# Performance work log

Measured on AMD Instinct MI355X. Metric: run time of the kernel, lower is better.

## Reference

```python
import jax, jax.numpy as jnp
import numpy as np

N_NODES = 20000
N_EDGES = 640000
HIDDEN = 128
HEADS = 8
HEAD_DIM = HIDDEN // HEADS
SCALE = HEAD_DIM ** -0.5
EPS = 1e-8


def setup_inputs() -> dict:
    key = jax.random.key(0)
    ks = jax.random.split(key, 12)
    s = HIDDEN ** -0.5
    return {
        "query": jax.random.normal(ks[0], (N_NODES, HIDDEN), jnp.float32),
        "key": jax.random.normal(ks[1], (N_NODES, HIDDEN), jnp.float32),
        "value": jax.random.normal(ks[2], (N_NODES, HIDDEN), jnp.float32),
        "edge_index": jax.random.randint(ks[3], (2, N_EDGES), 0, N_NODES, jnp.int64 if jax.config.jax_enable_x64 else jnp.int32),
        "Wq": jax.random.normal(ks[4], (HIDDEN, HIDDEN), jnp.float32) * s,
        "bq": jax.random.normal(ks[5], (HIDDEN,), jnp.float32) * s,
        "Wk": jax.random.normal(ks[6], (HIDDEN, HIDDEN), jnp.float32) * s,
        "bk": jax.random.normal(ks[7], (HIDDEN,), jnp.float32) * s,
        "Wv": jax.random.normal(ks[8], (HIDDEN, HIDDEN), jnp.float32) * s,
        "bv": jax.random.normal(ks[9], (HIDDEN,), jnp.float32) * s,
        "Wo": jax.random.normal(ks[10], (HIDDEN, HIDDEN), jnp.float32) * s,
        "bo": jax.random.normal(ks[11], (HIDDEN,), jnp.float32) * s,
    }


def reference(query, key, value, edge_index, Wq, bq, Wk, bk, Wv, bv, Wo, bo):
    n = query.shape[0]
    # projections (torch nn.Linear: x @ W.T + b)
    Q = (query @ Wq.T + bq).reshape(n, HEADS, HEAD_DIM)
    K = (key @ Wk.T + bk).reshape(n, HEADS, HEAD_DIM)
    V = (value @ Wv.T + bv).reshape(n, HEADS, HEAD_DIM)

    src, dst = edge_index[0], edge_index[1]
    # per-edge, per-head scores: [E, H]
    scores = jnp.einsum('ehd,ehd->eh', Q[dst], K[src]) * SCALE
    # segment softmax over incoming edges of each dst node
    seg_max = jax.ops.segment_max(scores, dst, num_segments=n)  # [N, H]
    seg_max = jnp.where(jnp.isfinite(seg_max), seg_max, 0.0)
    exp_scores = jnp.exp(scores - seg_max[dst])
    seg_sum = jax.ops.segment_sum(exp_scores, dst, num_segments=n)  # [N, H]
    attn = exp_scores / (seg_sum[dst] + EPS)  # [E, H]

    # scatter-weighted aggregation of V[src] into dst
    weighted = attn[:, :, None] * V[src]  # [E, H, D]
    out = jax.ops.segment_sum(weighted, dst, num_segments=n)  # [N, H, D]
    out = out.reshape(n, HIDDEN)
    return out @ Wo.T + bo
```

## Files before the change

kernel.cpp:

```cpp
#include <hip/hip_runtime.h>
#include <math.h>

#define NN 20000
#define NE 640000
#define HID 128
#define NH 8
#define HD 16
#define ATT_SCALE 0.25f

#define EPB 4096
#define NBLK1 157
#define NBUCK 157
#define SCAN_N (NBUCK * NBLK1)
#define SPT 25
#define PCHUNK 79

typedef __attribute__((ext_vector_type(8))) short bhalf8;
typedef __attribute__((ext_vector_type(4))) float floatx4;

#if defined(__has_builtin)
#if __has_builtin(__builtin_amdgcn_fdot2_f32_bf16)
#define USE_BF16_DOT2 1
#endif
#endif

__device__ __forceinline__ short f2b(float f) {
  union { float f; unsigned u; } a;
  a.f = f;
  unsigned r = a.u + 0x7FFF + ((a.u >> 16) & 1);
  return (short)(r >> 16);
}

__device__ __forceinline__ float b2f(short s) {
  union { unsigned u; float f; } a;
  a.u = ((unsigned)(unsigned short)s) << 16;
  return a.f;
}

#ifdef USE_BF16_DOT2
typedef __attribute__((ext_vector_type(2))) __bf16 bf16x2;
__device__ __forceinline__ bf16x2 asbf2(unsigned x) {
  union { unsigned u; bf16x2 v; } c;
  c.u = x;
  return c.v;
}
__device__ __forceinline__ float dot8(const bhalf8& k, const bhalf8& q) {
  const unsigned* kp = (const unsigned*)&k;
  const unsigned* qp = (const unsigned*)&q;
  float d = 0.f;
#pragma unroll
  for (int u = 0; u < 4; ++u)
    d = __builtin_amdgcn_fdot2_f32_bf16(asbf2(kp[u]), asbf2(qp[u]), d, false);
  return d;
}
#else
__device__ __forceinline__ float dot8(const bhalf8& k, const bhalf8& q) {
  float d = 0.f;
#pragma unroll
  for (int u = 0; u < 8; ++u) d += b2f(k[u]) * b2f(q[u]);
  return d;
}
#endif

__device__ __forceinline__ bhalf8 load_a8(const float* __restrict__ p) {
  float4 x0 = *(const float4*)p;
  float4 x1 = *(const float4*)(p + 4);
  bhalf8 a;
  a[0] = f2b(x0.x); a[1] = f2b(x0.y); a[2] = f2b(x0.z); a[3] = f2b(x0.w);
  a[4] = f2b(x1.x); a[5] = f2b(x1.y); a[6] = f2b(x1.z); a[7] = f2b(x1.w);
  return a;
}

__global__ __launch_bounds__(256) void k_hist_wconv(
    const int* __restrict__ dst, int* __restrict__ cnt1,
    const float* __restrict__ W0, const float* __restrict__ W1,
    const float* __restrict__ W2, const float* __restrict__ W3,
    short* __restrict__ out) {
  int t = threadIdx.x, b = blockIdx.x;
  if (b < NBLK1) {
    __shared__ int h[NBUCK];
    for (int i = t; i < NBUCK; i += 256) h[i] = 0;
    __syncthreads();
    const int4* d4 = (const int4*)dst;
    int q0 = (b * EPB) >> 2;
#pragma unroll
    for (int it = 0; it < EPB / 1024; ++it) {
      int i4 = q0 + it * 256 + t;
      if (i4 < NE / 4) {
        int4 d = d4[i4];
        atomicAdd(&h[d.x >> 7], 1);
        atomicAdd(&h[d.y >> 7], 1);
        atomicAdd(&h[d.z >> 7], 1);
        atomicAdd(&h[d.w >> 7], 1);
      }
    }
    __syncthreads();
    for (int i = t; i < NBUCK; i += 256) cnt1[i * NBLK1 + b] = h[i];
  } else {
    int i = (b - NBLK1) * 1024 + t * 4;
    int m = i >> 14;
    const float* src = (m == 0) ? W0 : (m == 1) ? W1 : (m == 2) ? W2 : W3;
    float4 x = *(const float4*)(src + (i & 16383));
    short4 o;
    o.x = f2b(x.x); o.y = f2b(x.y); o.z = f2b(x.z); o.w = f2b(x.w);
    *(short4*)(out + i) = o;
  }
}

template <int STRIDE, int HALF>
__device__ __forceinline__ void gemm_mfma(const float* __restrict__ X,
                                          const short* __restrict__ Wb,
                                          const float* __restrict__ B,
                                          short* __restrict__ O, int wrow) {
  int lane = threadIdx.x & 63;
  int rr = lane & 15;
  int g = lane >> 4;
  int arow = wrow + rr;
  floatx4 acc[8];
#pragma unroll
  for (int nt = 0; nt < 8; ++nt) acc[nt] = (floatx4){0.f, 0.f, 0.f, 0.f};
#pragma unroll
  for (int kt = 0; kt < 4; ++kt) {
    bhalf8 a;
    if (arow < NN) {
      a = load_a8(X + (size_t)arow * HID + kt * 32 + g * 8);
    } else {
      a = (bhalf8){0, 0, 0, 0, 0, 0, 0, 0};
    }
#pragma unroll
    for (int nt = 0; nt < 8; ++nt) {
      bhalf8 b = *(const bhalf8*)(Wb + (nt * 16 + rr) * HID + kt * 32 + g * 8);
      acc[nt] = __builtin_amdgcn_mfma_f32_16x16x32_bf16(a, b, acc[nt], 0, 0, 0);
    }
  }
  int orow0 = wrow + g * 4;
#pragma unroll
  for (int nt = 0; nt < 8; ++nt) {
    int col = nt * 16 + rr;
    float bias = B[col];
#pragma unroll
    for (int i = 0; i < 4; ++i) {
      int r = orow0 + i;
      if (r < NN) {
        O[((size_t)(nt >> 1) * NN + r) * STRIDE + HALF + (nt & 1) * 16 + rr] =
            f2b(acc[nt][i] + bias);
      }
    }
  }
}

__global__ __launch_bounds__(1024) void k_scan_proj(
    int* __restrict__ cnt1, int* __restrict__ boff,
    const float* __restrict__ q, const float* __restrict__ k,
    const float* __restrict__ v, const short* __restrict__ Wb,
    const float* __restrict__ bq, const float* __restrict__ bk,
    const float* __restrict__ bv, short* __restrict__ Qh,
    short* __restrict__ KVh) {
  __shared__ int sa[1024], sb[1024];
  int t = threadIdx.x;
  if (blockIdx.x == 0) {
    int base = t * SPT;
    int s = 0;
#pragma unroll 5
    for (int u = 0; u < SPT; ++u) {
      int i = base + u;
      s += (i < SCAN_N) ? cnt1[i] : 0;
    }
    sa[t] = s;
    __syncthreads();
    int* sp = sa;
    int* dp = sb;
    for (int st = 1; st < 1024; st <<= 1) {
      dp[t] = sp[t] + (t >= st ? sp[t - st] : 0);
      __syncthreads();
      int* tmp = sp; sp = dp; dp = tmp;
    }
    int run = sp[t] - s;
#pragma unroll 5
    for (int u = 0; u < SPT; ++u) {
      int i = base + u;
      if (i < SCAN_N) {
        int vv = cnt1[i];
        cnt1[i] = run;
        run += vv;
      }
    }
    __syncthreads();
    for (int i = t; i < NBUCK; i += 1024) boff[i] = cnt1[i * NBLK1];
    if (t == 0) boff[NBUCK] = NE;
  } else {
    int b = blockIdx.x - 1;
    int mat = b / PCHUNK;
    int wrow = (b % PCHUNK) * 256 + (t >> 6) * 16;
    if (mat == 0) gemm_mfma<32, 0>(q, Wb, bq, Qh, wrow);
    else if (mat == 1) gemm_mfma<64, 0>(k, Wb + 16384, bk, KVh, wrow);
    else gemm_mfma<64, 32>(v, Wb + 2 * 16384, bv, KVh, wrow);
  }
}

__global__ __launch_bounds__(256) void k_p1scat(const int* __restrict__ src,
                                                const int* __restrict__ dst,
                                                const int* __restrict__ cnt1,
                                                int* __restrict__ tmp) {
  __shared__ int cur[NBUCK];
  int t = threadIdx.x, b = blockIdx.x;
  for (int i = t; i < NBUCK; i += 256) cur[i] = cnt1[i * NBLK1 + b];
  __syncthreads();
  const int4* s4 = (const int4*)src;
  const int4* d4 = (const int4*)dst;
  int q0 = (b * EPB) >> 2;
#pragma unroll
  for (int it = 0; it < EPB / 1024; ++it) {
    int i4 = q0 + it * 256 + t;
    if (i4 < NE / 4) {
      int4 s = s4[i4];
      int4 d = d4[i4];
      int p;
      p = atomicAdd(&cur[d.x >> 7], 1); tmp[p] = (s.x << 7) | (d.x & 127);
      p = atomicAdd(&cur[d.y >> 7], 1); tmp[p] = (s.y << 7) | (d.y & 127);
      p = atomicAdd(&cur[d.z >> 7], 1); tmp[p] = (s.z << 7) | (d.z & 127);
      p = atomicAdd(&cur[d.w >> 7], 1); tmp[p] = (s.w << 7) | (d.w & 127);
    }
  }
}

__global__ __launch_bounds__(128, 4) void k_edge(
    const int* __restrict__ tmp, const int* __restrict__ boff,
    const short* __restrict__ Qh, const short* __restrict__ KVh,
    const short* __restrict__ Wb, const float* __restrict__ bo,
    float* __restrict__ O) {
  __shared__ int hits[512];
  __shared__ int els[512];
  __shared__ short att[8][136];
  __shared__ int h8[8], c8[8], o8[8];
  __shared__ int nhit;
  int t = threadIdx.x;
  int bx = blockIdx.x;
  int b = bx >> 4;
  int l0 = (bx & 15) * 8;
  int node0 = 8 * bx;
  if (t < 8) h8[t] = 0;
  if (t == 0) nhit = 0;
  __syncthreads();
  int lo = boff[b], hi = boff[b + 1];
  const int4* t4 = (const int4*)tmp;
  int q0i = lo >> 2, q1i = (hi + 3) >> 2;
  for (int i4 = q0i + t; i4 < q1i; i4 += 128) {
    int4 w4 = t4[i4];
    int e = 4 * i4;
#pragma unroll
    for (int u = 0; u < 4; ++u) {
      int w = (u == 0) ? w4.x : (u == 1) ? w4.y : (u == 2) ? w4.z : w4.w;
      int ei = e + u;
      if (ei >= lo && ei < hi) {
        unsigned rel = (unsigned)((w & 127) - l0);
        if (rel < 8u) {
          int p = atomicAdd(&nhit, 1);
          if (p < 512) hits[p] = w;
          atomicAdd(&h8[rel], 1);
        }
      }
    }
  }
  __syncthreads();
  if (t == 0) {
    int r = 0;
#pragma unroll
    for (int u = 0; u < 8; ++u) {
      o8[u] = r;
      c8[u] = r;
      r += h8[u];
    }
  }
  __syncthreads();
  int n = nhit < 512 ? nhit : 512;
  for (int i = t; i < n; i += 128) {
    int w = hits[i];
    int p = atomicAdd(&c8[(w & 127) - l0], 1);
    els[p] = w >> 7;
  }
  __syncthreads();
  int nl = t >> 4;
  int node = node0 + nl;
  int sub = t & 15;
  int j = sub >> 2;
  int r = sub & 3;
  int i0 = o8[nl];
  int i1 = i0 + h8[nl];
  bool valid = node < NN;
#pragma unroll
  for (int hp = 0; hp < 4; ++hp) {
    bhalf8 qv = (bhalf8){0, 0, 0, 0, 0, 0, 0, 0};
    if (valid)
      qv = *(const bhalf8*)(Qh + ((size_t)hp * NN + node) * 32 + r * 8);
    float l = 0.f;
    float acc[8];
#pragma unroll
    for (int u = 0; u < 8; ++u) acc[u] = 0.f;
    int i = i0 + j;
    for (; i + 4 < i1; i += 8) {
      int s1 = els[i], s2 = els[i + 4];
      const short* b1 = KVh + ((size_t)hp * NN + s1) * 64;
      const short* b2 = KVh + ((size_t)hp * NN + s2) * 64;
      bhalf8 kc1 = *(const bhalf8*)(b1 + r * 8);
      bhalf8 vc1 = *(const bhalf8*)(b1 + 32 + r * 8);
      bhalf8 kc2 = *(const bhalf8*)(b2 + r * 8);
      bhalf8 vc2 = *(const bhalf8*)(b2 + 32 + r * 8);
      float d1 = dot8(kc1, qv);
      float d2 = dot8(kc2, qv);
      d1 += __shfl_xor(d1, 1, 64);
      d2 += __shfl_xor(d2, 1, 64);
      float p1 = __expf(d1 * ATT_SCALE);
      float p2 = __expf(d2 * ATT_SCALE);
      l += p1 + p2;
#pragma unroll
      for (int u = 0; u < 8; ++u) acc[u] += p1 * b2f(vc1[u]) + p2 * b2f(vc2[u]);
    }
    if (i < i1) {
      int s1 = els[i];
      const short* b1 = KVh + ((size_t)hp * NN + s1) * 64;
      bhalf8 kc1 = *(const bhalf8*)(b1 + r * 8);
      bhalf8 vc1 = *(const bhalf8*)(b1 + 32 + r * 8);
      float d1 = dot8(kc1, qv);
      d1 += __shfl_xor(d1, 1, 64);
      float p1 = __expf(d1 * ATT_SCALE);
      l += p1;
#pragma unroll
      for (int u = 0; u < 8; ++u) acc[u] += p1 * b2f(vc1[u]);
    }
#pragma unroll
    for (int mask = 4; mask <= 8; mask <<= 1) {
      l += __shfl_xor(l, mask, 64);
#pragma unroll
      for (int u = 0; u < 8; ++u) acc[u] += __shfl_xor(acc[u], mask, 64);
    }
    float inv = 1.f / (l + 1e-8f);
    if (j == 0) {
      bhalf8 st;
#pragma unroll
      for (int u = 0; u < 8; ++u) st[u] = f2b(acc[u] * inv);
      *(bhalf8*)(&att[nl][hp * 32 + r * 8]) = st;
    }
  }
  __syncthreads();
  int w = t >> 6;
  int plane = t & 63;
  int rr = plane & 15;
  int pg = plane >> 4;
  const short* Wo = Wb + 3 * 16384;
  floatx4 oacc[4];
#pragma unroll
  for (int ntl = 0; ntl < 4; ++ntl) oacc[ntl] = (floatx4){0.f, 0.f, 0.f, 0.f};
#pragma unroll
  for (int kt = 0; kt < 4; ++kt) {
    bhalf8 a;
    if (rr < 8 && node0 + rr < NN) {
      a = *(const bhalf8*)(&att[rr][kt * 32 + pg * 8]);
    } else {
      a = (bhalf8){0, 0, 0, 0, 0, 0, 0, 0};
    }
#pragma unroll
    for (int ntl = 0; ntl < 4; ++ntl) {
      int nt = w * 4 + ntl;
      bhalf8 bb = *(const bhalf8*)(Wo + (nt * 16 + rr) * HID + kt * 32 + pg * 8);
      oacc[ntl] = __builtin_amdgcn_mfma_f32_16x16x32_bf16(a, bb, oacc[ntl], 0, 0, 0);
    }
  }
#pragma unroll
  for (int ntl = 0; ntl < 4; ++ntl) {
    int col = (w * 4 + ntl) * 16 + rr;
    float bias = bo[col];
#pragma unroll
    for (int ii = 0; ii < 4; ++ii) {
      int rw = pg * 4 + ii;
      if (rw < 8 && node0 + rw < NN) {
        O[(size_t)(node0 + rw) * HID + col] = oacc[ntl][ii] + bias;
      }
    }
  }
}

extern "C" void kernel_launch(void* const* d_in, const int* in_sizes, int n_in,
                              void* d_out, int out_size, void* d_ws,
                              size_t ws_size, hipStream_t stream) {
  const float* q = (const float*)d_in[0];
  const float* k = (const float*)d_in[1];
  const float* v = (const float*)d_in[2];
  const int* ei = (const int*)d_in[3];
  const float* Wq = (const float*)d_in[4];
  const float* bq = (const float*)d_in[5];
  const float* Wk = (const float*)d_in[6];
  const float* bk = (const float*)d_in[7];
  const float* Wv = (const float*)d_in[8];
  const float* bv = (const float*)d_in[9];
  const float* Wo = (const float*)d_in[10];
  const float* bo = (const float*)d_in[11];
  const int* src = ei;
  const int* dst = ei + NE;

  int* tmp = (int*)d_ws;
  int* cnt1 = tmp + NE;
  int* boff = cnt1 + 24704;
  short* Wb = (short*)(boff + 160);
  short* Qh = Wb + 4 * 16384;
  short* KVh = Qh + NN * HID;
  float* O = (float*)d_out;

  k_hist_wconv<<<NBLK1 + 64, 256, 0, stream>>>(dst, cnt1, Wq, Wk, Wv, Wo, Wb);
  k_scan_proj<<<1 + 3 * PCHUNK, 1024, 0, stream>>>(cnt1, boff, q, k, v, Wb, bq,
                                                   bk, bv, Qh, KVh);
  k_p1scat<<<NBLK1, 256, 0, stream>>>(src, dst, cnt1, tmp);
  k_edge<<<NBUCK * 16, 128, 0, stream>>>(tmp, boff, Qh, KVh, Wb, bo, O);
}
```

Measured before the change: 93.03 us.

## Fuse bucket scan into scatter blocks and merge with projection kernel

Removes the single-block global scan and the separate scatter launch. Each scatter block now recomputes its own bucket offsets by reading the histogram row per bucket and doing a 256-wide block scan, then scatters edges. These blocks run in the same launch as the projection GEMM blocks, which are re-chunked into 256-thread blocks of 64 rows. This drops one kernel launch and a serial scan dependency, at the cost of redundant histogram reads (157x157 per block).

```diff
diff --git a/kernel.cpp b/kernel.cpp
--- a/kernel.cpp
+++ b/kernel.cpp
@@ -11,9 +11,7 @@
 #define EPB 4096
 #define NBLK1 157
 #define NBUCK 157
-#define SCAN_N (NBUCK * NBLK1)
-#define SPT 25
-#define PCHUNK 79
+#define PCH64 313
 
 typedef __attribute__((ext_vector_type(8))) short bhalf8;
 typedef __attribute__((ext_vector_type(4))) float floatx4;
@@ -149,66 +147,54 @@
   }
 }
 
-__global__ __launch_bounds__(1024) void k_scan_proj(
-    int* __restrict__ cnt1, int* __restrict__ boff,
+__global__ __launch_bounds__(256) void k_proj_scat(
+    const int* __restrict__ cnt1, int* __restrict__ boff, int* __restrict__ tmp,
+    const int* __restrict__ esrc, const int* __restrict__ edst,
     const float* __restrict__ q, const float* __restrict__ k,
     const float* __restrict__ v, const short* __restrict__ Wb,
     const float* __restrict__ bq, const float* __restrict__ bk,
     const float* __restrict__ bv, short* __restrict__ Qh,
     short* __restrict__ KVh) {
-  __shared__ int sa[1024], sb[1024];
+  int b = blockIdx.x;
   int t = threadIdx.x;
-  if (blockIdx.x == 0) {
-    int base = t * SPT;
-    int s = 0;
-#pragma unroll 5
-    for (int u = 0; u < SPT; ++u) {
-      int i = base + u;
-      s += (i < SCAN_N) ? cnt1[i] : 0;
-    }
-    sa[t] = s;
-    __syncthreads();
-    int* sp = sa;
-    int* dp = sb;
-    for (int st = 1; st < 1024; st <<= 1) {
-      dp[t] = sp[t] + (t >= st ? sp[t - st] : 0);
-      __syncthreads();
-      int* tmp = sp; sp = dp; dp = tmp;
-    }
-    int run = sp[t] - s;
-#pragma unroll 5
-    for (int u = 0; u < SPT; ++u) {
-      int i = base + u;
-      if (i < SCAN_N) {
-        int vv = cnt1[i];
-        cnt1[i] = run;
-        run += vv;
-      }
-    }
-    __syncthreads();
-    for (int i = t; i < NBUCK; i += 1024) boff[i] = cnt1[i * NBLK1];
-    if (t == 0) boff[NBUCK] = NE;
-  } else {
-    int b = blockIdx.x - 1;
-    int mat = b / PCHUNK;
-    int wrow = (b % PCHUNK) * 256 + (t >> 6) * 16;
+  if (b < 3 * PCH64) {
+    int mat = b / PCH64;
+    int wrow = (b % PCH64) * 64 + (t >> 6) * 16;
     if (mat == 0) gemm_mfma<32, 0>(q, Wb, bq, Qh, wrow);
     else if (mat == 1) gemm_mfma<64, 0>(k, Wb + 16384, bk, KVh, wrow);
     else gemm_mfma<64, 32>(v, Wb + 2 * 16384, bv, KVh, wrow);
-  }
-}
-
-__global__ __launch_bounds__(256) void k_p1scat(const int* __restrict__ src,
-                                                const int* __restrict__ dst,
-                                                const int* __restrict__ cnt1,
-                                                int* __restrict__ tmp) {
-  __shared__ int cur[NBUCK];
-  int t = threadIdx.x, b = blockIdx.x;
-  for (int i = t; i < NBUCK; i += 256) cur[i] = cnt1[i * NBLK1 + b];
-  __syncthreads();
-  const int4* s4 = (const int4*)src;
-  const int4* d4 = (const int4*)dst;
-  int q0 = (b * EPB) >> 2;
+    return;
+  }
+  int sb = b - 3 * PCH64;
+  __shared__ int sA[256], sB[256], cur[NBUCK];
+  int rowtot = 0, rowpre = 0;
+  if (t < NBUCK) {
+    const int* row = cnt1 + t * NBLK1;
+    for (int blk = 0; blk < NBLK1; ++blk) {
+      int vv = row[blk];
+      rowtot += vv;
+      if (blk < sb) rowpre += vv;
+    }
+  }
+  sA[t] = (t < NBUCK) ? rowtot : 0;
+  __syncthreads();
+  int* sp = sA;
+  int* dp = sB;
+  for (int st = 1; st < 256; st <<= 1) {
+    dp[t] = sp[t] + (t >= st ? sp[t - st] : 0);
+    __syncthreads();
+    int* tm = sp; sp = dp; dp = tm;
+  }
+  int pre = sp[t] - ((t < NBUCK) ? rowtot : 0);
+  if (t < NBUCK) cur[t] = pre + rowpre;
+  if (sb == 0) {
+    if (t < NBUCK) boff[t] = pre;
+    if (t == 0) boff[NBUCK] = NE;
+  }
+  __syncthreads();
+  const int4* s4 = (const int4*)esrc;
+  const int4* d4 = (const int4*)edst;
+  int q0 = (sb * EPB) >> 2;
 #pragma unroll
   for (int it = 0; it < EPB / 1024; ++it) {
     int i4 = q0 + it * 256 + t;
@@ -407,8 +393,7 @@
   float* O = (float*)d_out;
 
   k_hist_wconv<<<NBLK1 + 64, 256, 0, stream>>>(dst, cnt1, Wq, Wk, Wv, Wo, Wb);
-  k_scan_proj<<<1 + 3 * PCHUNK, 1024, 0, stream>>>(cnt1, boff, q, k, v, Wb, bq,
-                                                   bk, bv, Qh, KVh);
-  k_p1scat<<<NBLK1, 256, 0, stream>>>(src, dst, cnt1, tmp);
+  k_proj_scat<<<3 * PCH64 + NBLK1, 256, 0, stream>>>(
+      cnt1, boff, tmp, src, dst, q, k, v, Wb, bq, bk, bv, Qh, KVh);
   k_edge<<<NBUCK * 16, 128, 0, stream>>>(tmp, boff, Qh, KVh, Wb, bo, O);
 }
```

Result: faster. 82.81 us (-11.0%).
